# Kernel optimization log

Hardware: AMD Instinct MI355X
Metric: run time of the kernel (lower is better)

The kernel has to match this reference:

```python
import jax, jax.numpy as jnp
import numpy as np

N_HEAD = 12
D_HEAD = 64  # inner_dim 768 / 12 heads

def quick_gelu(x):
    return x * jax.nn.sigmoid(1.702 * x)

def setup_inputs() -> dict:
    key = jax.random.key(0)
    ks = jax.random.split(key, 12)
    B, Nv, Lt, Cv, Ct, Ci = 256, 196, 32, 768, 512, 768
    s = lambda k, shp, fan: jax.random.normal(k, shp, jnp.float32) / np.sqrt(fan)
    return {
        "vis_tokens": jax.random.normal(ks[0], (B, Nv, Cv), jnp.float32),
        "text_tokens": jax.random.normal(ks[1], (B, Lt, Ct), jnp.float32),
        "Wq": s(ks[2], (Cv, Ci), Cv), "bq": jnp.zeros((Ci,), jnp.float32),
        "Wk": s(ks[3], (Ct, Ci), Ct), "bk": jnp.zeros((Ci,), jnp.float32),
        "Wv": s(ks[4], (Ct, Ci), Ct), "bv": jnp.zeros((Ci,), jnp.float32),
        "W1": s(ks[5], (Ci, Ci), Ci), "b1": jnp.zeros((Ci,), jnp.float32),
        "W2": s(ks[6], (Ci, 2), Ci), "b2": jnp.zeros((2,), jnp.float32),
    }

def reference(vis_tokens, text_tokens, Wq, bq, Wk, bk, Wv, bv, W1, b1, W2, b2):
    B, Nv, _ = vis_tokens.shape
    Lt = text_tokens.shape[1]
    Ci = Wq.shape[1]
    # projections -> [B, H, N, D]
    q = (vis_tokens @ Wq + bq).reshape(B, Nv, N_HEAD, D_HEAD).transpose(0, 2, 1, 3)
    k = (text_tokens @ Wk + bk).reshape(B, Lt, N_HEAD, D_HEAD).transpose(0, 2, 1, 3)
    v = (text_tokens @ Wv + bv).reshape(B, Lt, N_HEAD, D_HEAD).transpose(0, 2, 1, 3)
    scores = jnp.einsum('bhnd,bhld->bhnl', q, k) / np.sqrt(D_HEAD).astype(np.float32)
    attn = jax.nn.softmax(scores, axis=-1)           # [B,H,Nv,Lt]
    ctx = jnp.einsum('bhnl,bhld->bhnd', attn, v)      # [B,H,Nv,D]
    ctx = ctx.transpose(0, 2, 1, 3).reshape(B, Nv, Ci)
    fused = ctx + vis_tokens[..., :Ci]
    logits = quick_gelu(fused @ W1 + b1) @ W2 + b2    # [B,Nv,2]
    rel_BN = attn.mean(axis=-1).mean(axis=1)          # [B,Nv]
    return (logits, rel_BN)
```

## Files before the change

### kernel.cpp

```cpp
#include <hip/hip_runtime.h>
#include <hip/hip_bf16.h>


typedef __attribute__((ext_vector_type(8))) short bf16x8;
typedef __attribute__((ext_vector_type(4))) float f32x4;

__device__ __forceinline__ float bf2f(unsigned short u) {
    return __uint_as_float(((unsigned int)u) << 16);
}
__device__ __forceinline__ unsigned short f2bf(float f) {
    unsigned int x = __float_as_uint(f);
    unsigned int r = (x + 0x7FFFu + ((x >> 16) & 1u)) >> 16;
    return (unsigned short)r;
}

#define GLOAD_LDS16(gp, lp)                                                    \
    __builtin_amdgcn_global_load_lds(                                          \
        (__attribute__((address_space(1))) void*)(gp),                         \
        (__attribute__((address_space(3))) void*)(lp), 16, 0, 0)

#define BAR()  __builtin_amdgcn_s_barrier()
#define SCHED0 __builtin_amdgcn_sched_barrier(0)
#define VMC0  asm volatile("s_waitcnt vmcnt(0)" ::: "memory")
#define VMC8  asm volatile("s_waitcnt vmcnt(8)" ::: "memory")

__global__ void cvt2_kernel(const float* __restrict__ in0,
                            unsigned short* __restrict__ out0, int n0,
                            const float* __restrict__ in1,
                            unsigned short* __restrict__ out1) {
    int i = blockIdx.x * 256 + threadIdx.x;
    const float* in = in0; unsigned short* out = out0;
    if (i >= n0) { i -= n0; in = in1; out = out1; }
    float4 v = ((const float4*)in)[i];
    ushort4 o;
    o.x = f2bf(v.x); o.y = f2bf(v.y); o.z = f2bf(v.z); o.w = f2bf(v.w);
    ((ushort4*)out)[i] = o;
}

__global__ void transpose4_kernel(const float* __restrict__ Wq, unsigned short* __restrict__ Wqt,
                                  const float* __restrict__ Wk, unsigned short* __restrict__ Wkt,
                                  const float* __restrict__ Wv, unsigned short* __restrict__ Wvt,
                                  const float* __restrict__ W1, unsigned short* __restrict__ W1t) {
    __shared__ float tile[32][33];
    int id = blockIdx.x;
    const float* W; unsigned short* Wt; int K;
    if (id < 576)       { W = Wq; Wt = Wqt; K = 768; }
    else if (id < 960)  { id -= 576;  W = Wk; Wt = Wkt; K = 512; }
    else if (id < 1344) { id -= 960;  W = Wv; Wt = Wvt; K = 512; }
    else                { id -= 1344; W = W1; Wt = W1t; K = 768; }
    int n0 = (id % 24) * 32, k0 = (id / 24) * 32;
    int tx = threadIdx.x & 31, ty = threadIdx.x >> 5;
    #pragma unroll
    for (int r = ty; r < 32; r += 8)
        tile[r][tx] = W[(size_t)(k0 + r) * 768 + n0 + tx];
    __syncthreads();
    #pragma unroll
    for (int r = ty; r < 32; r += 8)
        Wt[(size_t)(n0 + r) * K + k0 + tx] = f2bf(tile[tx][r]);
}

template<int KTOT, int GELU, int MTILES>
__device__ __forceinline__
void gemm_body(int id, const unsigned short* __restrict__ A,
               const unsigned short* __restrict__ Bt,
               const float* __restrict__ bias,
               unsigned short* __restrict__ C,
               unsigned short* As, unsigned short* Bs) {
    constexpr int NT = KTOT / 64;
    constexpr int PAN = 4096;
    constexpr int TSZ = 2 * PAN;
    const int tid = threadIdx.x;
    const int lane = tid & 63, wave = tid >> 6;
    const int wm = (wave >> 1) * 64, wn = (wave & 1) * 64;
    const int lr = lane & 15, quad = lane >> 4;

    const int xcd = id & 7, local = id >> 3;
    const int nt = local % 6, mt = xcd * (MTILES / 8) + local / 6;
    const size_t m0 = (size_t)mt * 128;
    const int n0 = nt * 128;

    const int slotoff = ((quad ^ (((lr >> 3) & 1) << 1)) << 3);
    const int aBase = (wm + lr) * 32 + slotoff;
    const int bBase = (wn + lr) * 32 + slotoff;

    const int sg = (lane & 3) ^ (((lane >> 5) & 1) << 1);
    const unsigned short* gA = A + (m0 + (lane >> 2)) * (size_t)KTOT + sg * 8;
    const unsigned short* gB = Bt + ((size_t)n0 + (lane >> 2)) * KTOT + sg * 8;
    const int sr = wave * 32;

#define STG(b, t) do {                                                         \
    _Pragma("unroll")                                                          \
    for (int p_ = 0; p_ < 2; ++p_) {                                           \
        _Pragma("unroll")                                                      \
        for (int q_ = 0; q_ < 2; ++q_) {                                       \
            const int r0_ = sr + q_ * 16;                                      \
            GLOAD_LDS16(gA + (size_t)r0_ * KTOT + (t) * 64 + p_ * 32,          \
                        As + (b) * TSZ + p_ * PAN + r0_ * 32);                 \
            GLOAD_LDS16(gB + (size_t)r0_ * KTOT + (t) * 64 + p_ * 32,          \
                        Bs + (b) * TSZ + p_ * PAN + r0_ * 32);                 \
        }                                                                      \
    }                                                                          \
} while (0)

    f32x4 acc[4][4] = {};

#define COMPUTE(bsel) do {                                                     \
    const unsigned short* pa = As + (bsel) * TSZ;                              \
    const unsigned short* pb = Bs + (bsel) * TSZ;                              \
    _Pragma("unroll")                                                          \
    for (int kk = 0; kk < 2; ++kk) {                                           \
        bf16x8 fa[4], fb[4];                                                   \
        _Pragma("unroll")                                                      \
        for (int i = 0; i < 4; ++i)                                            \
            fa[i] = *(const bf16x8*)(pa + kk * PAN + aBase + i * 512);         \
        _Pragma("unroll")                                                      \
        for (int j = 0; j < 4; ++j)                                            \
            fb[j] = *(const bf16x8*)(pb + kk * PAN + bBase + j * 512);         \
        _Pragma("unroll")                                                      \
        for (int i = 0; i < 4; ++i)                                            \
            _Pragma("unroll")                                                  \
            for (int j = 0; j < 4; ++j)                                        \
                acc[i][j] = __builtin_amdgcn_mfma_f32_16x16x32_bf16(           \
                    fa[i], fb[j], acc[i][j], 0, 0, 0);                         \
    }                                                                          \
} while (0)

    STG(0, 0);
    STG(1, 1);
    VMC8;
    BAR(); SCHED0;

    for (int t = 0; t < NT - 1; ++t) {
        COMPUTE(t & 1);
        BAR(); SCHED0;
        if (t + 2 < NT) { STG(t & 1, t + 2); VMC8; }
        else            { VMC0; }
        BAR(); SCHED0;
    }
    COMPUTE((NT - 1) & 1);

    float bvv[4];
    #pragma unroll
    for (int j = 0; j < 4; ++j)
        bvv[j] = bias[n0 + wn + j * 16 + lr];
    #pragma unroll
    for (int i = 0; i < 4; ++i) {
        #pragma unroll
        for (int r2 = 0; r2 < 4; ++r2) {
            size_t row = m0 + wm + i * 16 + quad * 4 + r2;
            unsigned short* cp = C + row * 768 + n0 + wn + lr;
            #pragma unroll
            for (int j = 0; j < 4; ++j) {
                float x = acc[i][j][r2] + bvv[j];
                if (GELU) x = x / (1.0f + __expf(-1.702f * x));
                cp[j * 16] = f2bf(x);
            }
        }
    }
#undef STG
#undef COMPUTE
}

template<int KTOT, int GELU, int MTILES>
__global__ __launch_bounds__(256, 2)
void gemm_db_kernel(const unsigned short* __restrict__ A,
                    const unsigned short* __restrict__ Bt,
                    const float* __restrict__ bias,
                    unsigned short* __restrict__ C) {
    __shared__ unsigned short As[2 * 8192];
    __shared__ unsigned short Bs[2 * 8192];
    gemm_body<KTOT, GELU, MTILES>(blockIdx.x, A, Bt, bias, C, As, Bs);
}

template<int KTOT, int MTILES>
__global__ __launch_bounds__(256, 2)
void gemm_kv_kernel(const unsigned short* __restrict__ A,
                    const unsigned short* __restrict__ Bt0,
                    const float* __restrict__ bias0,
                    unsigned short* __restrict__ C0,
                    const unsigned short* __restrict__ Bt1,
                    const float* __restrict__ bias1,
                    unsigned short* __restrict__ C1) {
    __shared__ unsigned short As[2 * 8192];
    __shared__ unsigned short Bs[2 * 8192];
    const int half = gridDim.x >> 1;
    if (blockIdx.x < half)
        gemm_body<KTOT, 0, MTILES>(blockIdx.x, A, Bt0, bias0, C0, As, Bs);
    else
        gemm_body<KTOT, 0, MTILES>(blockIdx.x - half, A, Bt1, bias1, C1, As, Bs);
}

__global__ __launch_bounds__(256, 4)
void attn_mfma_kernel(const unsigned short* __restrict__ Q,
                      const unsigned short* __restrict__ Kb,
                      const unsigned short* __restrict__ Vb,
                      unsigned short* __restrict__ RF) {
    constexpr int KS = 72;
    constexpr int VS = 34;
    constexpr int PS = 40;
    constexpr int CS = 72;
    __shared__ unsigned short Ks[32 * KS];
    __shared__ unsigned short Vt[64 * VS];
    __shared__ unsigned short Pb[4][16 * PS];
    __shared__ unsigned short Cb[4][16 * CS];
    const int tid = threadIdx.x;
    const int b = blockIdx.x / 12, h = blockIdx.x % 12;
    const int lane = tid & 63, wave = tid >> 6;
    const int lr = lane & 15, quad = lane >> 4;

    {
        int l = tid >> 3, d8 = (tid & 7) * 8;
        size_t base = ((size_t)b * 32 + l) * 768 + (size_t)h * 64 + d8;
        bf16x8 kv = *(const bf16x8*)(Kb + base);
        bf16x8 vv = *(const bf16x8*)(Vb + base);
        *(bf16x8*)(Ks + l * KS + d8) = kv;
        #pragma unroll
        for (int j = 0; j < 8; ++j)
            Vt[(d8 + j) * VS + l] = (unsigned short)vv[j];
    }
    __syncthreads();

    bf16x8 fbK[2][2];
    #pragma unroll
    for (int n = 0; n < 2; ++n)
        #pragma unroll
        for (int ks = 0; ks < 2; ++ks)
            fbK[n][ks] = *(const bf16x8*)(Ks + (n * 16 + lr) * KS + ks * 32 + quad * 8);
    bf16x8 fbV[4];
    #pragma unroll
    for (int d = 0; d < 4; ++d)
        fbV[d] = *(const bf16x8*)(Vt + (d * 16 + lr) * VS + quad * 8);

    const size_t qbase = (size_t)b * 196 * 768 + (size_t)h * 64;

    for (int t = wave; t < 13; t += 4) {
        const int m0 = t * 16;
        int qrow = m0 + lr; if (qrow > 195) qrow = 195;
        const unsigned short* qp = Q + qbase + (size_t)qrow * 768;
        bf16x8 fa0 = *(const bf16x8*)(qp + quad * 8);
        bf16x8 fa1 = *(const bf16x8*)(qp + 32 + quad * 8);
        f32x4 s0 = {}, s1 = {};
        s0 = __builtin_amdgcn_mfma_f32_16x16x32_bf16(fa0, fbK[0][0], s0, 0, 0, 0);
        s0 = __builtin_amdgcn_mfma_f32_16x16x32_bf16(fa1, fbK[0][1], s0, 0, 0, 0);
        s1 = __builtin_amdgcn_mfma_f32_16x16x32_bf16(fa0, fbK[1][0], s1, 0, 0, 0);
        s1 = __builtin_amdgcn_mfma_f32_16x16x32_bf16(fa1, fbK[1][1], s1, 0, 0, 0);

        float p0[4], p1[4], m4[4], s4[4];
        #pragma unroll
        for (int r = 0; r < 4; ++r) {
            p0[r] = s0[r] * 0.125f;
            p1[r] = s1[r] * 0.125f;
            m4[r] = fmaxf(p0[r], p1[r]);
        }
        #pragma unroll
        for (int off = 1; off < 16; off <<= 1)
            #pragma unroll
            for (int r = 0; r < 4; ++r)
                m4[r] = fmaxf(m4[r], __shfl_xor(m4[r], off));
        #pragma unroll
        for (int r = 0; r < 4; ++r) {
            p0[r] = __expf(p0[r] - m4[r]);
            p1[r] = __expf(p1[r] - m4[r]);
            s4[r] = p0[r] + p1[r];
        }
        #pragma unroll
        for (int off = 1; off < 16; off <<= 1)
            #pragma unroll
            for (int r = 0; r < 4; ++r)
                s4[r] += __shfl_xor(s4[r], off);
        #pragma unroll
        for (int r = 0; r < 4; ++r) {
            float inv = __builtin_amdgcn_rcpf(s4[r]);
            unsigned short* pr = &Pb[wave][(quad * 4 + r) * PS];
            pr[lr]      = f2bf(p0[r] * inv);
            pr[16 + lr] = f2bf(p1[r] * inv);
        }

        bf16x8 fap = *(const bf16x8*)(&Pb[wave][lr * PS + quad * 8]);
        f32x4 c[4];
        #pragma unroll
        for (int d = 0; d < 4; ++d) {
            f32x4 z = {};
            c[d] = __builtin_amdgcn_mfma_f32_16x16x32_bf16(fap, fbV[d], z, 0, 0, 0);
        }
        #pragma unroll
        for (int d = 0; d < 4; ++d)
            #pragma unroll
            for (int r = 0; r < 4; ++r)
                Cb[wave][(quad * 4 + r) * CS + d * 16 + lr] = f2bf(c[d][r]);
        #pragma unroll
        for (int i = 0; i < 2; ++i) {
            int c2 = lane + i * 64;
            int row = c2 >> 3, col8 = (c2 & 7) * 8;
            int grow = m0 + row;
            if (grow < 196) {
                bf16x8 cv = *(const bf16x8*)(&Cb[wave][row * CS + col8]);
                unsigned short* gp = RF + qbase + (size_t)grow * 768 + col8;
                bf16x8 rv = *(const bf16x8*)gp;
                bf16x8 ov;
                #pragma unroll
                for (int j = 0; j < 8; ++j)
                    ov[j] = (short)f2bf(bf2f((unsigned short)cv[j]) +
                                        bf2f((unsigned short)rv[j]));
                *(bf16x8*)gp = ov;
            }
        }
    }
}

__global__ __launch_bounds__(256)
void mlp2_kernel(const unsigned short* __restrict__ Hb,
                 const float* __restrict__ W2,
                 const float* __restrict__ b2,
                 float* __restrict__ out) {
    __shared__ float w2s[2][768];
    const int tid = threadIdx.x;
    for (int i = tid; i < 1536; i += 256) w2s[i & 1][i >> 1] = W2[i];
    __syncthreads();
    const int sub = tid & 7;
    const int r = tid >> 3;
    const size_t row = (size_t)blockIdx.x * 32 + r;
    float a0 = 0.f, a1 = 0.f;
    #pragma unroll
    for (int i = 0; i < 12; ++i) {
        int base = i * 64 + sub * 8;
        bf16x8 hv = *(const bf16x8*)(Hb + row * 768 + base);
        #pragma unroll
        for (int j = 0; j < 8; ++j) {
            float hf = bf2f((unsigned short)hv[j]);
            a0 += hf * w2s[0][base + j];
            a1 += hf * w2s[1][base + j];
        }
    }
    #pragma unroll
    for (int o = 4; o >= 1; o >>= 1) {
        a0 += __shfl_down(a0, o, 8);
        a1 += __shfl_down(a1, o, 8);
    }
    if (sub == 0) {
        out[row * 2]      = a0 + b2[0];
        out[row * 2 + 1]  = a1 + b2[1];
        out[100352 + row] = 0.03125f;
    }
}

extern "C" void kernel_launch(void* const* d_in, const int* in_sizes, int n_in,
                              void* d_out, int out_size, void* d_ws, size_t ws_size,
                              hipStream_t stream) {
    const float* vis = (const float*)d_in[0];
    const float* txt = (const float*)d_in[1];
    const float* Wq  = (const float*)d_in[2];
    const float* bq  = (const float*)d_in[3];
    const float* Wk  = (const float*)d_in[4];
    const float* bk  = (const float*)d_in[5];
    const float* Wv  = (const float*)d_in[6];
    const float* bv  = (const float*)d_in[7];
    const float* W1  = (const float*)d_in[8];
    const float* b1  = (const float*)d_in[9];
    const float* W2  = (const float*)d_in[10];
    const float* b2  = (const float*)d_in[11];
    float* out = (float*)d_out;

    char* w = (char*)d_ws;
    unsigned short* Abf = (unsigned short*)(w);
    unsigned short* Tbf = (unsigned short*)(w + 77070336);
    unsigned short* Wqt = (unsigned short*)(w + 85458944);
    unsigned short* Wkt = (unsigned short*)(w + 86638592);
    unsigned short* Wvt = (unsigned short*)(w + 87425024);
    unsigned short* W1t = (unsigned short*)(w + 88211456);
    unsigned short* Qbf = (unsigned short*)(w + 89391104);
    unsigned short* Kbf = (unsigned short*)(w + 166461440);
    unsigned short* Vbf = (unsigned short*)(w + 179044352);
    unsigned short* Hbf = Qbf;

    cvt2_kernel<<<41728, 256, 0, stream>>>(vis, Abf, 9633792, txt, Tbf);
    transpose4_kernel<<<1920, 256, 0, stream>>>(Wq, Wqt, Wk, Wkt, Wv, Wvt, W1, W1t);

    gemm_db_kernel<768, 0, 392><<<2352, 256, 0, stream>>>(Abf, Wqt, bq, Qbf);
    gemm_kv_kernel<512, 64><<<768, 256, 0, stream>>>(Tbf, Wkt, bk, Kbf, Wvt, bv, Vbf);

    attn_mfma_kernel<<<3072, 256, 0, stream>>>(Qbf, Kbf, Vbf, Abf);

    gemm_db_kernel<768, 1, 392><<<2352, 256, 0, stream>>>(Abf, W1t, b1, Hbf);

    mlp2_kernel<<<1568, 256, 0, stream>>>(Hbf, W2, b2, out);
}
```

Baseline: 511.2 us.

## Replace double-buffered GEMM pipeline with single-buffer loop; prefetch residual in attention

The GEMM main loop drops its two-stage LDS double buffering with explicit vmcnt waits in favour of a single buffer: each k-step loads, synchronizes, computes and synchronizes again. LDS usage is halved and launch bounds rise to 4 blocks per CU, trading in-block load/compute overlap for higher occupancy and overlap across blocks. Separately, the attention kernel now issues its residual loads before the QK MFMAs so their latency hides behind compute. The risk is exposed global-load latency in each GEMM iteration.

```diff
diff --git a/kernel.cpp b/kernel.cpp
--- a/kernel.cpp
+++ b/kernel.cpp
@@ -18,11 +18,6 @@
     __builtin_amdgcn_global_load_lds(                                          \
         (__attribute__((address_space(1))) void*)(gp),                         \
         (__attribute__((address_space(3))) void*)(lp), 16, 0, 0)
-
-#define BAR()  __builtin_amdgcn_s_barrier()
-#define SCHED0 __builtin_amdgcn_sched_barrier(0)
-#define VMC0  asm volatile("s_waitcnt vmcnt(0)" ::: "memory")
-#define VMC8  asm volatile("s_waitcnt vmcnt(8)" ::: "memory")
 
 __global__ void cvt2_kernel(const float* __restrict__ in0,
                             unsigned short* __restrict__ out0, int n0,
@@ -68,7 +63,6 @@
                unsigned short* As, unsigned short* Bs) {
     constexpr int NT = KTOT / 64;
     constexpr int PAN = 4096;
-    constexpr int TSZ = 2 * PAN;
     const int tid = threadIdx.x;
     const int lane = tid & 63, wave = tid >> 6;
     const int wm = (wave >> 1) * 64, wn = (wave & 1) * 64;
@@ -88,56 +82,39 @@
     const unsigned short* gB = Bt + ((size_t)n0 + (lane >> 2)) * KTOT + sg * 8;
     const int sr = wave * 32;
 
-#define STG(b, t) do {                                                         \
-    _Pragma("unroll")                                                          \
-    for (int p_ = 0; p_ < 2; ++p_) {                                           \
-        _Pragma("unroll")                                                      \
-        for (int q_ = 0; q_ < 2; ++q_) {                                       \
-            const int r0_ = sr + q_ * 16;                                      \
-            GLOAD_LDS16(gA + (size_t)r0_ * KTOT + (t) * 64 + p_ * 32,          \
-                        As + (b) * TSZ + p_ * PAN + r0_ * 32);                 \
-            GLOAD_LDS16(gB + (size_t)r0_ * KTOT + (t) * 64 + p_ * 32,          \
-                        Bs + (b) * TSZ + p_ * PAN + r0_ * 32);                 \
-        }                                                                      \
-    }                                                                          \
-} while (0)
-
     f32x4 acc[4][4] = {};
 
-#define COMPUTE(bsel) do {                                                     \
-    const unsigned short* pa = As + (bsel) * TSZ;                              \
-    const unsigned short* pb = Bs + (bsel) * TSZ;                              \
-    _Pragma("unroll")                                                          \
-    for (int kk = 0; kk < 2; ++kk) {                                           \
-        bf16x8 fa[4], fb[4];                                                   \
-        _Pragma("unroll")                                                      \
-        for (int i = 0; i < 4; ++i)                                            \
-            fa[i] = *(const bf16x8*)(pa + kk * PAN + aBase + i * 512);         \
-        _Pragma("unroll")                                                      \
-        for (int j = 0; j < 4; ++j)                                            \
-            fb[j] = *(const bf16x8*)(pb + kk * PAN + bBase + j * 512);         \
-        _Pragma("unroll")                                                      \
-        for (int i = 0; i < 4; ++i)                                            \
-            _Pragma("unroll")                                                  \
-            for (int j = 0; j < 4; ++j)                                        \
-                acc[i][j] = __builtin_amdgcn_mfma_f32_16x16x32_bf16(           \
-                    fa[i], fb[j], acc[i][j], 0, 0, 0);                         \
-    }                                                                          \
-} while (0)
-
-    STG(0, 0);
-    STG(1, 1);
-    VMC8;
-    BAR(); SCHED0;
-
-    for (int t = 0; t < NT - 1; ++t) {
-        COMPUTE(t & 1);
-        BAR(); SCHED0;
-        if (t + 2 < NT) { STG(t & 1, t + 2); VMC8; }
-        else            { VMC0; }
-        BAR(); SCHED0;
-    }
-    COMPUTE((NT - 1) & 1);
+    for (int t = 0; t < NT; ++t) {
+        #pragma unroll
+        for (int p = 0; p < 2; ++p) {
+            #pragma unroll
+            for (int q = 0; q < 2; ++q) {
+                const int r0 = sr + q * 16;
+                GLOAD_LDS16(gA + (size_t)r0 * KTOT + t * 64 + p * 32,
+                            As + p * PAN + r0 * 32);
+                GLOAD_LDS16(gB + (size_t)r0 * KTOT + t * 64 + p * 32,
+                            Bs + p * PAN + r0 * 32);
+            }
+        }
+        __syncthreads();
+        #pragma unroll
+        for (int kk = 0; kk < 2; ++kk) {
+            bf16x8 fa[4], fb[4];
+            #pragma unroll
+            for (int i = 0; i < 4; ++i)
+                fa[i] = *(const bf16x8*)(As + kk * PAN + aBase + i * 512);
+            #pragma unroll
+            for (int j = 0; j < 4; ++j)
+                fb[j] = *(const bf16x8*)(Bs + kk * PAN + bBase + j * 512);
+            #pragma unroll
+            for (int i = 0; i < 4; ++i)
+                #pragma unroll
+                for (int j = 0; j < 4; ++j)
+                    acc[i][j] = __builtin_amdgcn_mfma_f32_16x16x32_bf16(
+                        fa[i], fb[j], acc[i][j], 0, 0, 0);
+        }
+        __syncthreads();
+    }
 
     float bvv[4];
     #pragma unroll
@@ -157,23 +134,21 @@
             }
         }
     }
-#undef STG
-#undef COMPUTE
 }
 
 template<int KTOT, int GELU, int MTILES>
-__global__ __launch_bounds__(256, 2)
+__global__ __launch_bounds__(256, 4)
 void gemm_db_kernel(const unsigned short* __restrict__ A,
                     const unsigned short* __restrict__ Bt,
                     const float* __restrict__ bias,
                     unsigned short* __restrict__ C) {
-    __shared__ unsigned short As[2 * 8192];
-    __shared__ unsigned short Bs[2 * 8192];
+    __shared__ unsigned short As[2 * 4096];
+    __shared__ unsigned short Bs[2 * 4096];
     gemm_body<KTOT, GELU, MTILES>(blockIdx.x, A, Bt, bias, C, As, Bs);
 }
 
 template<int KTOT, int MTILES>
-__global__ __launch_bounds__(256, 2)
+__global__ __launch_bounds__(256, 4)
 void gemm_kv_kernel(const unsigned short* __restrict__ A,
                     const unsigned short* __restrict__ Bt0,
                     const float* __restrict__ bias0,
@@ -181,8 +156,8 @@
                     const unsigned short* __restrict__ Bt1,
                     const float* __restrict__ bias1,
                     unsigned short* __restrict__ C1) {
-    __shared__ unsigned short As[2 * 8192];
-    __shared__ unsigned short Bs[2 * 8192];
+    __shared__ unsigned short As[2 * 4096];
+    __shared__ unsigned short Bs[2 * 4096];
     const int half = gridDim.x >> 1;
     if (blockIdx.x < half)
         gemm_body<KTOT, 0, MTILES>(blockIdx.x, A, Bt0, bias0, C0, As, Bs);
@@ -239,6 +214,17 @@
         const unsigned short* qp = Q + qbase + (size_t)qrow * 768;
         bf16x8 fa0 = *(const bf16x8*)(qp + quad * 8);
         bf16x8 fa1 = *(const bf16x8*)(qp + 32 + quad * 8);
+
+        bf16x8 rv[2]; int rrow[2];
+        #pragma unroll
+        for (int i = 0; i < 2; ++i) {
+            int c2 = lane + i * 64;
+            rrow[i] = m0 + (c2 >> 3);
+            if (rrow[i] < 196)
+                rv[i] = *(const bf16x8*)(RF + qbase + (size_t)rrow[i] * 768 +
+                                         (c2 & 7) * 8);
+        }
+
         f32x4 s0 = {}, s1 = {};
         s0 = __builtin_amdgcn_mfma_f32_16x16x32_bf16(fa0, fbK[0][0], s0, 0, 0, 0);
         s0 = __builtin_amdgcn_mfma_f32_16x16x32_bf16(fa1, fbK[0][1], s0, 0, 0, 0);
@@ -292,16 +278,14 @@
         for (int i = 0; i < 2; ++i) {
             int c2 = lane + i * 64;
             int row = c2 >> 3, col8 = (c2 & 7) * 8;
-            int grow = m0 + row;
-            if (grow < 196) {
+            if (rrow[i] < 196) {
                 bf16x8 cv = *(const bf16x8*)(&Cb[wave][row * CS + col8]);
-                unsigned short* gp = RF + qbase + (size_t)grow * 768 + col8;
-                bf16x8 rv = *(const bf16x8*)gp;
+                unsigned short* gp = RF + qbase + (size_t)rrow[i] * 768 + col8;
                 bf16x8 ov;
                 #pragma unroll
                 for (int j = 0; j < 8; ++j)
                     ov[j] = (short)f2bf(bf2f((unsigned short)cv[j]) +
-                                        bf2f((unsigned short)rv[j]));
+                                        bf2f((unsigned short)rv[i][j]));
                 *(bf16x8*)gp = ov;
             }
         }
```

Result: faster. 488.7 us (-4.4%).
